# Kernel optimization log

Hardware: AMD Instinct MI355X
Metric: run time of the kernel (lower is better)

The kernel has to match this reference:

```python
import jax, jax.numpy as jnp
import numpy as np

N_NODES = 100000
N_EDGES = 1600000
IN_DIM = 64
HID = 128
N_CLASSES = 1
N_GRAPHS = 512


def _glorot(key, shape):
    fan_in, fan_out = shape[0], shape[1]
    lim = (6.0 / (fan_in + fan_out)) ** 0.5
    return jax.random.uniform(key, shape, jnp.float32, -lim, lim)


def setup_inputs() -> dict:
    key = jax.random.key(0)
    ks = jax.random.split(key, 10)
    x = jax.random.normal(ks[0], (N_NODES, IN_DIM), jnp.float32)
    edge_src = jax.random.randint(ks[1], (N_EDGES,), 0, N_NODES)
    edge_dst = jax.random.randint(ks[2], (N_EDGES,), 0, N_NODES)
    graph_ids = jnp.sort(jax.random.randint(ks[3], (N_NODES,), 0, N_GRAPHS))
    return {
        "x": x,
        "edge_src": edge_src,
        "edge_dst": edge_dst,
        "graph_ids": graph_ids,
        "W1": _glorot(ks[4], (IN_DIM, HID)),
        "b1": jnp.zeros((HID,), jnp.float32),
        "W2": _glorot(ks[5], (HID, HID)),
        "b2": jnp.zeros((HID,), jnp.float32),
        "Wc1": _glorot(ks[6], (HID, HID)),
        "bc1": jnp.zeros((HID,), jnp.float32),
        "Wc2": _glorot(ks[7], (HID, HID)),
        "bc2": jnp.zeros((HID,), jnp.float32),
        "Wc3": _glorot(ks[8], (HID, N_CLASSES)),
        "bc3": jnp.zeros((N_CLASSES,), jnp.float32),
    }


def _graph_conv(h, edge_src, edge_dst, W, b):
    # DGL GraphConv, norm='both': out = D_out^{-1/2} A D_in^{-1/2} h W + b
    ones = jnp.ones((edge_src.shape[0],), h.dtype)
    deg_out = jnp.clip(jax.ops.segment_sum(ones, edge_src, num_segments=N_NODES), 1.0)
    deg_in = jnp.clip(jax.ops.segment_sum(ones, edge_dst, num_segments=N_NODES), 1.0)
    h = h * jax.lax.rsqrt(deg_out)[:, None]           # src-side norm
    agg = jax.ops.segment_sum(h[edge_src], edge_dst, num_segments=N_NODES)  # [N, D]
    agg = agg * jax.lax.rsqrt(deg_in)[:, None]        # dst-side norm
    return agg @ W + b


def reference(x, edge_src, edge_dst, graph_ids, W1, b1, W2, b2, Wc1, bc1, Wc2, bc2, Wc3, bc3):
    h = jax.nn.relu(_graph_conv(x, edge_src, edge_dst, W1, b1))
    h = jax.nn.relu(_graph_conv(h, edge_src, edge_dst, W2, b2))
    # mean_nodes pooling over batched graphs
    sums = jax.ops.segment_sum(h, graph_ids, num_segments=N_GRAPHS)  # [G, H]
    cnts = jax.ops.segment_sum(jnp.ones((N_NODES,), h.dtype), graph_ids, num_segments=N_GRAPHS)
    hg = sums / jnp.clip(cnts, 1.0)[:, None]
    out = jax.nn.relu(hg @ Wc1 + bc1)
    out = jax.nn.relu(out @ Wc2 + bc2)
    return out @ Wc3 + bc3  # [G, n_classes]
```

## Files before the change

### kernel.cpp

```cpp
#include <hip/hip_runtime.h>

#define N_NODES 100000
#define N_EDGES 1600000
#define IN_DIM 64
#define HID 128
#define N_GRAPHS 512
#define NBUCK 391

__global__ __launch_bounds__(256) void k_bhist(const int* __restrict__ src, const int* __restrict__ dst,
                                               int* __restrict__ dcnt, int* __restrict__ scnt) {
    __shared__ int hd[NBUCK];
    __shared__ int hs[NBUCK];
    const int t = threadIdx.x;
    const int e0 = blockIdx.x * 4096 + t * 16;
    for (int i = t; i < NBUCK; i += 256) { hd[i] = 0; hs[i] = 0; }
    __syncthreads();
    if (e0 < N_EDGES) {
        const int4* d4 = (const int4*)(dst + e0);
        const int4* s4 = (const int4*)(src + e0);
#pragma unroll
        for (int u = 0; u < 4; ++u) {
            int4 d = d4[u], s = s4[u];
            atomicAdd(&hd[d.x >> 8], 1); atomicAdd(&hd[d.y >> 8], 1);
            atomicAdd(&hd[d.z >> 8], 1); atomicAdd(&hd[d.w >> 8], 1);
            atomicAdd(&hs[s.x >> 8], 1); atomicAdd(&hs[s.y >> 8], 1);
            atomicAdd(&hs[s.z >> 8], 1); atomicAdd(&hs[s.w >> 8], 1);
        }
    }
    __syncthreads();
    for (int i = t; i < NBUCK; i += 256) {
        if (hd[i]) atomicAdd(&dcnt[i], hd[i]);
        if (hs[i]) atomicAdd(&scnt[i], hs[i]);
    }
}

__global__ __launch_bounds__(512) void k_bscan3(const int* __restrict__ dcnt, const int* __restrict__ scnt,
                                                const int* __restrict__ gid,
                                                int* __restrict__ dbase, int* __restrict__ sbase,
                                                int* __restrict__ dcur, int* __restrict__ scur,
                                                int* __restrict__ gstart) {
    const int t = threadIdx.x;
    if (blockIdx.x == 2) {
        for (int g = t; g <= N_GRAPHS; g += 512) {
            int lo = 0, hi = N_NODES;
            while (lo < hi) {
                int mid = (lo + hi) >> 1;
                if (gid[mid] < g) lo = mid + 1; else hi = mid;
            }
            gstart[g] = lo;
        }
        return;
    }
    __shared__ int l[512];
    const int* cntp = (blockIdx.x == 0) ? dcnt : scnt;
    int* basep = (blockIdx.x == 0) ? dbase : sbase;
    int* curp  = (blockIdx.x == 0) ? dcur  : scur;
    int v = (t < NBUCK) ? cntp[t] : 0;
    l[t] = v;
    __syncthreads();
    for (int off = 1; off < 512; off <<= 1) {
        int x = (t >= off) ? l[t - off] : 0;
        __syncthreads();
        l[t] += x;
        __syncthreads();
    }
    if (t < NBUCK) {
        int excl = l[t] - v;
        basep[t] = excl; curp[t] = excl;
    }
    if (t == NBUCK - 1) basep[NBUCK] = l[t];
}

__global__ __launch_bounds__(256) void k_bin2(const int* __restrict__ src, const int* __restrict__ dst,
                                              int* __restrict__ dcur, int* __restrict__ scur,
                                              int* __restrict__ binnedD, int* __restrict__ binnedS) {
    __shared__ int hd[NBUCK];
    __shared__ int bd[NBUCK];
    __shared__ int hs[NBUCK];
    __shared__ int bs[NBUCK];
    const int t = threadIdx.x;
    const int e0 = blockIdx.x * 4096 + t * 16;
    for (int i = t; i < NBUCK; i += 256) { hd[i] = 0; hs[i] = 0; }
    __syncthreads();
    if (e0 < N_EDGES) {
        const int4* d4 = (const int4*)(dst + e0);
        const int4* s4 = (const int4*)(src + e0);
#pragma unroll
        for (int u = 0; u < 4; ++u) {
            int4 d = d4[u], s = s4[u];
            atomicAdd(&hd[d.x >> 8], 1); atomicAdd(&hd[d.y >> 8], 1);
            atomicAdd(&hd[d.z >> 8], 1); atomicAdd(&hd[d.w >> 8], 1);
            atomicAdd(&hs[s.x >> 8], 1); atomicAdd(&hs[s.y >> 8], 1);
            atomicAdd(&hs[s.z >> 8], 1); atomicAdd(&hs[s.w >> 8], 1);
        }
    }
    __syncthreads();
    for (int i = t; i < NBUCK; i += 256) {
        int c = hd[i];
        bd[i] = c ? atomicAdd(&dcur[i], c) : 0;
        hd[i] = 0;
        c = hs[i];
        bs[i] = c ? atomicAdd(&scur[i], c) : 0;
        hs[i] = 0;
    }
    __syncthreads();
    if (e0 < N_EDGES) {
        const int4* d4 = (const int4*)(dst + e0);
        const int4* s4 = (const int4*)(src + e0);
#pragma unroll
        for (int u = 0; u < 4; ++u) {
            int4 d = d4[u];
            int4 s = s4[u];
            int bk, r;
            bk = d.x >> 8; r = atomicAdd(&hd[bk], 1); binnedD[bd[bk] + r] = s.x | ((d.x & 255) << 17);
            bk = d.y >> 8; r = atomicAdd(&hd[bk], 1); binnedD[bd[bk] + r] = s.y | ((d.y & 255) << 17);
            bk = d.z >> 8; r = atomicAdd(&hd[bk], 1); binnedD[bd[bk] + r] = s.z | ((d.z & 255) << 17);
            bk = d.w >> 8; r = atomicAdd(&hd[bk], 1); binnedD[bd[bk] + r] = s.w | ((d.w & 255) << 17);
            bk = s.x >> 8; r = atomicAdd(&hs[bk], 1); binnedS[bs[bk] + r] = s.x;
            bk = s.y >> 8; r = atomicAdd(&hs[bk], 1); binnedS[bs[bk] + r] = s.y;
            bk = s.z >> 8; r = atomicAdd(&hs[bk], 1); binnedS[bs[bk] + r] = s.z;
            bk = s.w >> 8; r = atomicAdd(&hs[bk], 1); binnedS[bs[bk] + r] = s.w;
        }
    }
}

__global__ __launch_bounds__(256) void k_prep2(const int* __restrict__ dbase, const int* __restrict__ sbase,
                                               const int* __restrict__ binnedD, const int* __restrict__ binnedS,
                                               int* __restrict__ rowp, float* __restrict__ rsi,
                                               float* __restrict__ rso, int* __restrict__ col) {
    const int t = threadIdx.x;
    if (blockIdx.x < NBUCK) {
        const int b = blockIdx.x;
        const int n0 = b * 256;
        __shared__ int cnt[256];
        __shared__ int scn[256];
        __shared__ int cur[256];
        __shared__ int sb[2];
        if (t < 2) sb[t] = dbase[b + t];
        cnt[t] = 0;
        __syncthreads();
        const int s = sb[0], e = sb[1];
        for (int i = s + t; i < e; i += 256) atomicAdd(&cnt[binnedD[i] >> 17], 1);
        __syncthreads();
        const int c = cnt[t];
        scn[t] = c;
        __syncthreads();
        for (int off = 1; off < 256; off <<= 1) {
            int v = (t >= off) ? scn[t - off] : 0;
            __syncthreads();
            scn[t] += v;
            __syncthreads();
        }
        const int excl = scn[t] - c;
        cur[t] = excl;
        if (n0 + t < N_NODES) {
            rowp[n0 + t] = s + excl;
            rsi[n0 + t] = 1.0f / sqrtf(fmaxf((float)c, 1.0f));
        }
        if (b == NBUCK - 1 && t == 0) rowp[N_NODES] = e;
        __syncthreads();
        for (int i = s + t; i < e; i += 256) {
            int p = binnedD[i];
            int r = atomicAdd(&cur[p >> 17], 1);
            col[s + r] = p & 0x1FFFF;
        }
    } else {
        const int b = blockIdx.x - NBUCK;
        const int n0 = b * 256;
        __shared__ int cnt2[256];
        __shared__ int sb2[2];
        if (t < 2) sb2[t] = sbase[b + t];
        cnt2[t] = 0;
        __syncthreads();
        const int s = sb2[0], e = sb2[1];
        for (int i = s + t; i < e; i += 256) atomicAdd(&cnt2[binnedS[i] - n0], 1);
        __syncthreads();
        if (n0 + t < N_NODES) rso[n0 + t] = 1.0f / sqrtf(fmaxf((float)cnt2[t], 1.0f));
    }
}

__global__ __launch_bounds__(256) void k_gather64(const float4* __restrict__ x4, const float* __restrict__ rso,
                                                  const int* __restrict__ rowp, const int* __restrict__ col,
                                                  float4* __restrict__ agg4) {
    int wv = (blockIdx.x * 256 + threadIdx.x) >> 6;
    if (wv >= N_NODES) return;
    int lane = threadIdx.x & 63;
    int grp = lane >> 4, li = lane & 15;
    int s = rowp[wv], e = rowp[wv + 1];
    float ax = 0.f, ay = 0.f, az = 0.f, aw = 0.f;
    int i = s + grp;
    for (; i + 12 < e; i += 16) {
        int c0 = col[i], c1 = col[i + 4], c2 = col[i + 8], c3 = col[i + 12];
        float4 v0 = x4[c0 * 16 + li];
        float4 v1 = x4[c1 * 16 + li];
        float4 v2 = x4[c2 * 16 + li];
        float4 v3 = x4[c3 * 16 + li];
        float r0 = rso[c0], r1 = rso[c1], r2 = rso[c2], r3 = rso[c3];
        ax = fmaf(r0, v0.x, ax); ay = fmaf(r0, v0.y, ay); az = fmaf(r0, v0.z, az); aw = fmaf(r0, v0.w, aw);
        ax = fmaf(r1, v1.x, ax); ay = fmaf(r1, v1.y, ay); az = fmaf(r1, v1.z, az); aw = fmaf(r1, v1.w, aw);
        ax = fmaf(r2, v2.x, ax); ay = fmaf(r2, v2.y, ay); az = fmaf(r2, v2.z, az); aw = fmaf(r2, v2.w, aw);
        ax = fmaf(r3, v3.x, ax); ay = fmaf(r3, v3.y, ay); az = fmaf(r3, v3.z, az); aw = fmaf(r3, v3.w, aw);
    }
    for (; i + 4 < e; i += 8) {
        int c0 = col[i], c1 = col[i + 4];
        float4 v0 = x4[c0 * 16 + li];
        float4 v1 = x4[c1 * 16 + li];
        float r0 = rso[c0], r1 = rso[c1];
        ax = fmaf(r0, v0.x, ax); ay = fmaf(r0, v0.y, ay); az = fmaf(r0, v0.z, az); aw = fmaf(r0, v0.w, aw);
        ax = fmaf(r1, v1.x, ax); ay = fmaf(r1, v1.y, ay); az = fmaf(r1, v1.z, az); aw = fmaf(r1, v1.w, aw);
    }
    for (; i < e; i += 4) {
        int c = col[i];
        float4 v = x4[c * 16 + li];
        float r = rso[c];
        ax = fmaf(r, v.x, ax); ay = fmaf(r, v.y, ay); az = fmaf(r, v.z, az); aw = fmaf(r, v.w, aw);
    }
    ax += __shfl_xor(ax, 16, 64); ay += __shfl_xor(ay, 16, 64);
    az += __shfl_xor(az, 16, 64); aw += __shfl_xor(aw, 16, 64);
    ax += __shfl_xor(ax, 32, 64); ay += __shfl_xor(ay, 32, 64);
    az += __shfl_xor(az, 32, 64); aw += __shfl_xor(aw, 32, 64);
    if (lane < 16) {
        float4 o; o.x = ax; o.y = ay; o.z = az; o.w = aw;
        agg4[wv * 16 + li] = o;
    }
}

__global__ __launch_bounds__(256) void k_gather128(const float4* __restrict__ h4, const int* __restrict__ rowp,
                                                   const int* __restrict__ col, float4* __restrict__ agg4) {
    int wv = (blockIdx.x * 256 + threadIdx.x) >> 6;
    if (wv >= N_NODES) return;
    int lane = threadIdx.x & 63;
    int grp = lane >> 5, li = lane & 31;
    int s = rowp[wv], e = rowp[wv + 1];
    float ax = 0.f, ay = 0.f, az = 0.f, aw = 0.f;
    int i = s + grp;
    for (; i + 14 < e; i += 16) {
        int c0 = col[i],      c1 = col[i + 2],  c2 = col[i + 4],  c3 = col[i + 6];
        int c4 = col[i + 8],  c5 = col[i + 10], c6 = col[i + 12], c7 = col[i + 14];
        float4 v0 = h4[c0 * 32 + li];
        float4 v1 = h4[c1 * 32 + li];
        float4 v2 = h4[c2 * 32 + li];
        float4 v3 = h4[c3 * 32 + li];
        float4 v4 = h4[c4 * 32 + li];
        float4 v5 = h4[c5 * 32 + li];
        float4 v6 = h4[c6 * 32 + li];
        float4 v7 = h4[c7 * 32 + li];
        ax += (v0.x + v1.x) + (v2.x + v3.x) + ((v4.x + v5.x) + (v6.x + v7.x));
        ay += (v0.y + v1.y) + (v2.y + v3.y) + ((v4.y + v5.y) + (v6.y + v7.y));
        az += (v0.z + v1.z) + (v2.z + v3.z) + ((v4.z + v5.z) + (v6.z + v7.z));
        aw += (v0.w + v1.w) + (v2.w + v3.w) + ((v4.w + v5.w) + (v6.w + v7.w));
    }
    for (; i + 6 < e; i += 8) {
        int c0 = col[i], c1 = col[i + 2], c2 = col[i + 4], c3 = col[i + 6];
        float4 v0 = h4[c0 * 32 + li];
        float4 v1 = h4[c1 * 32 + li];
        float4 v2 = h4[c2 * 32 + li];
        float4 v3 = h4[c3 * 32 + li];
        ax += v0.x + v1.x + v2.x + v3.x;
        ay += v0.y + v1.y + v2.y + v3.y;
        az += v0.z + v1.z + v2.z + v3.z;
        aw += v0.w + v1.w + v2.w + v3.w;
    }
    for (; i < e; i += 2) {
        float4 v = h4[col[i] * 32 + li];
        ax += v.x; ay += v.y; az += v.z; aw += v.w;
    }
    ax += __shfl_xor(ax, 32, 64); ay += __shfl_xor(ay, 32, 64);
    az += __shfl_xor(az, 32, 64); aw += __shfl_xor(aw, 32, 64);
    if (lane < 32) {
        float4 o; o.x = ax; o.y = ay; o.z = az; o.w = aw;
        agg4[wv * 32 + li] = o;
    }
}

template <int K, bool SCALE_OUT>
__global__ __launch_bounds__(256) void k_mm(const float* __restrict__ A, const float* __restrict__ W,
                                            const float* __restrict__ bias, const float* __restrict__ rsi,
                                            const float* __restrict__ rso, float* __restrict__ out) {
    __shared__ float WL[32 * 128];
    __shared__ float aL[64][33];
    const int t = threadIdx.x;
    const int jq = t & 31;
    const int ns = t >> 5;
    const int n0 = blockIdx.x * 64;
    float acc[8][4] = {};
    for (int kc = 0; kc < K; kc += 32) {
        const float4* Wg = (const float4*)(W + kc * 128);
        float4* WL4 = (float4*)WL;
#pragma unroll
        for (int u = 0; u < 4; ++u) WL4[t + 256 * u] = Wg[t + 256 * u];
        {
            int r = t >> 2, q = t & 3;
            int node = n0 + r;
#pragma unroll
            for (int h = 0; h < 2; ++h) {
                int qq = q + h * 4;
                float4 v = make_float4(0.f, 0.f, 0.f, 0.f);
                if (node < N_NODES) v = *(const float4*)(A + (size_t)node * K + kc + qq * 4);
                aL[r][qq * 4 + 0] = v.x; aL[r][qq * 4 + 1] = v.y;
                aL[r][qq * 4 + 2] = v.z; aL[r][qq * 4 + 3] = v.w;
            }
        }
        __syncthreads();
#pragma unroll
        for (int k = 0; k < 32; ++k) {
            float4 wv = ((const float4*)WL)[k * 32 + jq];
#pragma unroll
            for (int i = 0; i < 8; ++i) {
                float av = aL[ns * 8 + i][k];
                acc[i][0] += av * wv.x; acc[i][1] += av * wv.y;
                acc[i][2] += av * wv.z; acc[i][3] += av * wv.w;
            }
        }
        __syncthreads();
    }
#pragma unroll
    for (int i = 0; i < 8; ++i) {
        int node = n0 + ns * 8 + i;
        if (node >= N_NODES) continue;
        float ri = rsi[node];
        float ro = SCALE_OUT ? rso[node] : 1.0f;
        float4 bj = ((const float4*)bias)[jq];
        float4 o;
        o.x = fmaxf(acc[i][0] * ri + bj.x, 0.f) * ro;
        o.y = fmaxf(acc[i][1] * ri + bj.y, 0.f) * ro;
        o.z = fmaxf(acc[i][2] * ri + bj.z, 0.f) * ro;
        o.w = fmaxf(acc[i][3] * ri + bj.w, 0.f) * ro;
        *(float4*)(out + node * HID + jq * 4) = o;
    }
}

__global__ __launch_bounds__(256) void k_mm2pool(const float* __restrict__ A, const float* __restrict__ W,
                                                 const float* __restrict__ bias, const float* __restrict__ rsi,
                                                 const int* __restrict__ gid, float* __restrict__ gsum) {
    __shared__ float WL[32 * 128];
    __shared__ float aL[64][33];
    __shared__ float gpart[8][128];
    const int t = threadIdx.x;
    const int jq = t & 31;
    const int ns = t >> 5;
    const int n0 = blockIdx.x * 64;
    for (int u = t; u < 8 * 128; u += 256) ((float*)gpart)[u] = 0.f;
    float acc[8][4] = {};
    for (int kc = 0; kc < HID; kc += 32) {
        const float4* Wg = (const float4*)(W + kc * 128);
        float4* WL4 = (float4*)WL;
#pragma unroll
        for (int u = 0; u < 4; ++u) WL4[t + 256 * u] = Wg[t + 256 * u];
        {
            int r = t >> 2, q = t & 3;
            int node = n0 + r;
#pragma unroll
            for (int h = 0; h < 2; ++h) {
                int qq = q + h * 4;
                float4 v = make_float4(0.f, 0.f, 0.f, 0.f);
                if (node < N_NODES) v = *(const float4*)(A + (size_t)node * HID + kc + qq * 4);
                aL[r][qq * 4 + 0] = v.x; aL[r][qq * 4 + 1] = v.y;
                aL[r][qq * 4 + 2] = v.z; aL[r][qq * 4 + 3] = v.w;
            }
        }
        __syncthreads();
#pragma unroll
        for (int k = 0; k < 32; ++k) {
            float4 wv = ((const float4*)WL)[k * 32 + jq];
#pragma unroll
            for (int i = 0; i < 8; ++i) {
                float av = aL[ns * 8 + i][k];
                acc[i][0] += av * wv.x; acc[i][1] += av * wv.y;
                acc[i][2] += av * wv.z; acc[i][3] += av * wv.w;
            }
        }
        __syncthreads();
    }
    const int g0 = gid[n0];
    float4 bj = ((const float4*)bias)[jq];
    int curslot = -9;
    float p0 = 0.f, p1 = 0.f, p2 = 0.f, p3 = 0.f;
#pragma unroll
    for (int i = 0; i < 8; ++i) {
        int node = n0 + ns * 8 + i;
        if (node >= N_NODES) break;
        float ri = rsi[node];
        float ox = fmaxf(acc[i][0] * ri + bj.x, 0.f);
        float oy = fmaxf(acc[i][1] * ri + bj.y, 0.f);
        float oz = fmaxf(acc[i][2] * ri + bj.z, 0.f);
        float ow = fmaxf(acc[i][3] * ri + bj.w, 0.f);
        int slot = gid[node] - g0;
        if (slot != curslot) {
            if (curslot >= 0) {
                if (curslot < 8) {
                    atomicAdd(&gpart[curslot][jq * 4 + 0], p0);
                    atomicAdd(&gpart[curslot][jq * 4 + 1], p1);
                    atomicAdd(&gpart[curslot][jq * 4 + 2], p2);
                    atomicAdd(&gpart[curslot][jq * 4 + 3], p3);
                } else {
                    atomicAdd(&gsum[(g0 + curslot) * HID + jq * 4 + 0], p0);
                    atomicAdd(&gsum[(g0 + curslot) * HID + jq * 4 + 1], p1);
                    atomicAdd(&gsum[(g0 + curslot) * HID + jq * 4 + 2], p2);
                    atomicAdd(&gsum[(g0 + curslot) * HID + jq * 4 + 3], p3);
                }
            }
            curslot = slot; p0 = ox; p1 = oy; p2 = oz; p3 = ow;
        } else {
            p0 += ox; p1 += oy; p2 += oz; p3 += ow;
        }
    }
    if (curslot >= 0) {
        if (curslot < 8) {
            atomicAdd(&gpart[curslot][jq * 4 + 0], p0);
            atomicAdd(&gpart[curslot][jq * 4 + 1], p1);
            atomicAdd(&gpart[curslot][jq * 4 + 2], p2);
            atomicAdd(&gpart[curslot][jq * 4 + 3], p3);
        } else {
            atomicAdd(&gsum[(g0 + curslot) * HID + jq * 4 + 0], p0);
            atomicAdd(&gsum[(g0 + curslot) * HID + jq * 4 + 1], p1);
            atomicAdd(&gsum[(g0 + curslot) * HID + jq * 4 + 2], p2);
            atomicAdd(&gsum[(g0 + curslot) * HID + jq * 4 + 3], p3);
        }
    }
    __syncthreads();
    for (int u = t; u < 8 * 128; u += 256) {
        int slot = u >> 7, c = u & 127;
        float v = gpart[slot][c];
        if (v != 0.f) {
            int g = g0 + slot;
            if (g < N_GRAPHS) atomicAdd(&gsum[g * HID + c], v);
        }
    }
}

__global__ __launch_bounds__(128) void k_head(const float* __restrict__ gsum, const int* __restrict__ gstart,
                                              const float* __restrict__ Wc1, const float* __restrict__ bc1,
                                              const float* __restrict__ Wc2, const float* __restrict__ bc2,
                                              const float* __restrict__ Wc3, const float* __restrict__ bc3,
                                              float* __restrict__ out) {
    int g = blockIdx.x, t = threadIdx.x;
    int s = gstart[g], e = gstart[g + 1];
    float cnt = fmaxf((float)(e - s), 1.0f);
    __shared__ float buf[HID];
    __shared__ float red[2];
    buf[t] = gsum[g * HID + t] / cnt;
    __syncthreads();
    float a = bc1[t];
#pragma unroll 8
    for (int k = 0; k < HID; ++k) a += buf[k] * Wc1[k * HID + t];
    a = fmaxf(a, 0.f);
    __syncthreads();
    buf[t] = a;
    __syncthreads();
    float b = bc2[t];
#pragma unroll 8
    for (int k = 0; k < HID; ++k) b += buf[k] * Wc2[k * HID + t];
    b = fmaxf(b, 0.f);
    float p = b * Wc3[t];
    for (int off = 32; off > 0; off >>= 1) p += __shfl_down(p, off, 64);
    if ((t & 63) == 0) red[t >> 6] = p;
    __syncthreads();
    if (t == 0) out[g] = red[0] + red[1] + bc3[0];
}

extern "C" void kernel_launch(void* const* d_in, const int* in_sizes, int n_in,
                              void* d_out, int out_size, void* d_ws, size_t ws_size,
                              hipStream_t stream) {
    const float* x   = (const float*)d_in[0];
    const int* esrc  = (const int*)d_in[1];
    const int* edst  = (const int*)d_in[2];
    const int* gid   = (const int*)d_in[3];
    const float* W1  = (const float*)d_in[4];
    const float* b1  = (const float*)d_in[5];
    const float* W2  = (const float*)d_in[6];
    const float* b2  = (const float*)d_in[7];
    const float* Wc1 = (const float*)d_in[8];
    const float* bc1 = (const float*)d_in[9];
    const float* Wc2 = (const float*)d_in[10];
    const float* bc2 = (const float*)d_in[11];
    const float* Wc3 = (const float*)d_in[12];
    const float* bc3 = (const float*)d_in[13];
    float* out = (float*)d_out;

    char* w = (char*)d_ws;
    size_t off = 0;
    auto alloc = [&](size_t bytes) -> char* {
        char* p = w + off;
        off += (bytes + 255) & ~(size_t)255;
        return p;
    };
    int* dcnt   = (int*)alloc((size_t)2 * (NBUCK + 1) * 4);
    int* scnt   = dcnt + (NBUCK + 1);
    int* dbase  = (int*)alloc((size_t)(NBUCK + 1) * 4);
    int* sbase  = (int*)alloc((size_t)(NBUCK + 1) * 4);
    int* dcur   = (int*)alloc((size_t)NBUCK * 4);
    int* scur   = (int*)alloc((size_t)NBUCK * 4);
    float* rso  = (float*)alloc((size_t)N_NODES * 4);
    float* rsi  = (float*)alloc((size_t)N_NODES * 4);
    int* rowp   = (int*)alloc((size_t)(N_NODES + 1) * 4);
    int* gstart = (int*)alloc((size_t)(N_GRAPHS + 1) * 4);
    int* col    = (int*)alloc((size_t)N_EDGES * 4);
    float* gsum = (float*)alloc((size_t)N_GRAPHS * HID * 4);
    float* R1   = (float*)alloc((size_t)N_NODES * HID * 4);
    float* R2   = (float*)alloc((size_t)N_NODES * HID * 4);
    int* binnedD = (int*)R1;
    int* binnedS = (int*)R1 + (size_t)N_EDGES;
    float* agg1 = R1;
    float* agg2 = R1;
    float* h1s  = R2;

    (void)in_sizes; (void)n_in; (void)out_size; (void)ws_size;

    hipMemsetAsync(dcnt, 0, (size_t)2 * (NBUCK + 1) * 4, stream);
    hipMemsetAsync(gsum, 0, (size_t)N_GRAPHS * HID * 4, stream);

    const int BB = (N_EDGES + 4095) / 4096;
    const int GB = (N_NODES * 64 + 255) / 256;
    const int MB64 = (N_NODES + 63) / 64;

    k_bhist<<<BB, 256, 0, stream>>>(esrc, edst, dcnt, scnt);
    k_bscan3<<<3, 512, 0, stream>>>(dcnt, scnt, gid, dbase, sbase, dcur, scur, gstart);
    k_bin2<<<BB, 256, 0, stream>>>(esrc, edst, dcur, scur, binnedD, binnedS);
    k_prep2<<<2 * NBUCK, 256, 0, stream>>>(dbase, sbase, binnedD, binnedS, rowp, rsi, rso, col);
    k_gather64<<<GB, 256, 0, stream>>>((const float4*)x, rso, rowp, col, (float4*)agg1);
    k_mm<IN_DIM, true><<<MB64, 256, 0, stream>>>(agg1, W1, b1, rsi, rso, h1s);
    k_gather128<<<GB, 256, 0, stream>>>((const float4*)h1s, rowp, col, (float4*)agg2);
    k_mm2pool<<<MB64, 256, 0, stream>>>(agg2, W2, b2, rsi, gid, gsum);
    k_head<<<N_GRAPHS, 128, 0, stream>>>(gsum, gstart, Wc1, bc1, Wc2, bc2, Wc3, bc3, out);
}
```

Measured before the change: 350.1 us.

## Fuse layer-2 neighbor gather into matmul+pooling kernel via shared memory

Merges the 128-wide gather kernel with the second matmul and mean-pooling kernel. Each 256-thread block now gathers 32 nodes into shared memory and runs the GEMM straight from there. This removes the global write and re-read of the 100000x128 aggregation buffer and one kernel launch. In exchange, each block runs only 4 waves of gather work with a shared-memory barrier before the GEMM, the 16-wide unrolled gather is dropped, and the tile shrinks to 32 nodes, which doubles the number of W2 reloads into shared memory.

```diff
diff --git a/kernel.cpp b/kernel.cpp
--- a/kernel.cpp
+++ b/kernel.cpp
@@ -225,54 +225,6 @@
     }
 }
 
-__global__ __launch_bounds__(256) void k_gather128(const float4* __restrict__ h4, const int* __restrict__ rowp,
-                                                   const int* __restrict__ col, float4* __restrict__ agg4) {
-    int wv = (blockIdx.x * 256 + threadIdx.x) >> 6;
-    if (wv >= N_NODES) return;
-    int lane = threadIdx.x & 63;
-    int grp = lane >> 5, li = lane & 31;
-    int s = rowp[wv], e = rowp[wv + 1];
-    float ax = 0.f, ay = 0.f, az = 0.f, aw = 0.f;
-    int i = s + grp;
-    for (; i + 14 < e; i += 16) {
-        int c0 = col[i],      c1 = col[i + 2],  c2 = col[i + 4],  c3 = col[i + 6];
-        int c4 = col[i + 8],  c5 = col[i + 10], c6 = col[i + 12], c7 = col[i + 14];
-        float4 v0 = h4[c0 * 32 + li];
-        float4 v1 = h4[c1 * 32 + li];
-        float4 v2 = h4[c2 * 32 + li];
-        float4 v3 = h4[c3 * 32 + li];
-        float4 v4 = h4[c4 * 32 + li];
-        float4 v5 = h4[c5 * 32 + li];
-        float4 v6 = h4[c6 * 32 + li];
-        float4 v7 = h4[c7 * 32 + li];
-        ax += (v0.x + v1.x) + (v2.x + v3.x) + ((v4.x + v5.x) + (v6.x + v7.x));
-        ay += (v0.y + v1.y) + (v2.y + v3.y) + ((v4.y + v5.y) + (v6.y + v7.y));
-        az += (v0.z + v1.z) + (v2.z + v3.z) + ((v4.z + v5.z) + (v6.z + v7.z));
-        aw += (v0.w + v1.w) + (v2.w + v3.w) + ((v4.w + v5.w) + (v6.w + v7.w));
-    }
-    for (; i + 6 < e; i += 8) {
-        int c0 = col[i], c1 = col[i + 2], c2 = col[i + 4], c3 = col[i + 6];
-        float4 v0 = h4[c0 * 32 + li];
-        float4 v1 = h4[c1 * 32 + li];
-        float4 v2 = h4[c2 * 32 + li];
-        float4 v3 = h4[c3 * 32 + li];
-        ax += v0.x + v1.x + v2.x + v3.x;
-        ay += v0.y + v1.y + v2.y + v3.y;
-        az += v0.z + v1.z + v2.z + v3.z;
-        aw += v0.w + v1.w + v2.w + v3.w;
-    }
-    for (; i < e; i += 2) {
-        float4 v = h4[col[i] * 32 + li];
-        ax += v.x; ay += v.y; az += v.z; aw += v.w;
-    }
-    ax += __shfl_xor(ax, 32, 64); ay += __shfl_xor(ay, 32, 64);
-    az += __shfl_xor(az, 32, 64); aw += __shfl_xor(aw, 32, 64);
-    if (lane < 32) {
-        float4 o; o.x = ax; o.y = ay; o.z = az; o.w = aw;
-        agg4[wv * 32 + li] = o;
-    }
-}
-
 template <int K, bool SCALE_OUT>
 __global__ __launch_bounds__(256) void k_mm(const float* __restrict__ A, const float* __restrict__ W,
                                             const float* __restrict__ bias, const float* __restrict__ rsi,
@@ -330,56 +282,78 @@
     }
 }
 
-__global__ __launch_bounds__(256) void k_mm2pool(const float* __restrict__ A, const float* __restrict__ W,
-                                                 const float* __restrict__ bias, const float* __restrict__ rsi,
-                                                 const int* __restrict__ gid, float* __restrict__ gsum) {
+__global__ __launch_bounds__(256, 4) void k_g128p(const float4* __restrict__ h4, const int* __restrict__ rowp,
+                                                  const int* __restrict__ col, const float* __restrict__ W,
+                                                  const float* __restrict__ bias, const float* __restrict__ rsi,
+                                                  const int* __restrict__ gid, float* __restrict__ gsum) {
+    __shared__ float agg[32][HID];
     __shared__ float WL[32 * 128];
-    __shared__ float aL[64][33];
     __shared__ float gpart[8][128];
     const int t = threadIdx.x;
+    const int wid = t >> 6, lane = t & 63;
+    const int n0 = blockIdx.x * 32;
+    for (int u = t; u < 8 * 128; u += 256) ((float*)gpart)[u] = 0.f;
+
+    const int grp = lane >> 5, li = lane & 31;
+#pragma unroll 1
+    for (int it = 0; it < 8; ++it) {
+        const int node = n0 + wid * 8 + it;
+        const int s = rowp[node], e = rowp[node + 1];
+        float ax = 0.f, ay = 0.f, az = 0.f, aw = 0.f;
+        int i = s + grp;
+        for (; i + 6 < e; i += 8) {
+            int c0 = col[i], c1 = col[i + 2], c2 = col[i + 4], c3 = col[i + 6];
+            float4 v0 = h4[c0 * 32 + li];
+            float4 v1 = h4[c1 * 32 + li];
+            float4 v2 = h4[c2 * 32 + li];
+            float4 v3 = h4[c3 * 32 + li];
+            ax += v0.x + v1.x + v2.x + v3.x;
+            ay += v0.y + v1.y + v2.y + v3.y;
+            az += v0.z + v1.z + v2.z + v3.z;
+            aw += v0.w + v1.w + v2.w + v3.w;
+        }
+        for (; i < e; i += 2) {
+            float4 v = h4[col[i] * 32 + li];
+            ax += v.x; ay += v.y; az += v.z; aw += v.w;
+        }
+        ax += __shfl_xor(ax, 32, 64); ay += __shfl_xor(ay, 32, 64);
+        az += __shfl_xor(az, 32, 64); aw += __shfl_xor(aw, 32, 64);
+        if (lane < 32) {
+            float4 o; o.x = ax; o.y = ay; o.z = az; o.w = aw;
+            ((float4*)agg[node - n0])[li] = o;
+        }
+    }
+    __syncthreads();
+
     const int jq = t & 31;
     const int ns = t >> 5;
-    const int n0 = blockIdx.x * 64;
-    for (int u = t; u < 8 * 128; u += 256) ((float*)gpart)[u] = 0.f;
-    float acc[8][4] = {};
+    float acc[4][4] = {};
     for (int kc = 0; kc < HID; kc += 32) {
         const float4* Wg = (const float4*)(W + kc * 128);
         float4* WL4 = (float4*)WL;
 #pragma unroll
         for (int u = 0; u < 4; ++u) WL4[t + 256 * u] = Wg[t + 256 * u];
-        {
-            int r = t >> 2, q = t & 3;
-            int node = n0 + r;
-#pragma unroll
-            for (int h = 0; h < 2; ++h) {
-                int qq = q + h * 4;
-                float4 v = make_float4(0.f, 0.f, 0.f, 0.f);
-                if (node < N_NODES) v = *(const float4*)(A + (size_t)node * HID + kc + qq * 4);
-                aL[r][qq * 4 + 0] = v.x; aL[r][qq * 4 + 1] = v.y;
-                aL[r][qq * 4 + 2] = v.z; aL[r][qq * 4 + 3] = v.w;
-            }
-        }
         __syncthreads();
 #pragma unroll
         for (int k = 0; k < 32; ++k) {
             float4 wv = ((const float4*)WL)[k * 32 + jq];
 #pragma unroll
-            for (int i = 0; i < 8; ++i) {
-                float av = aL[ns * 8 + i][k];
+            for (int i = 0; i < 4; ++i) {
+                float av = agg[ns * 4 + i][kc + k];
                 acc[i][0] += av * wv.x; acc[i][1] += av * wv.y;
                 acc[i][2] += av * wv.z; acc[i][3] += av * wv.w;
             }
         }
         __syncthreads();
     }
+
     const int g0 = gid[n0];
     float4 bj = ((const float4*)bias)[jq];
     int curslot = -9;
     float p0 = 0.f, p1 = 0.f, p2 = 0.f, p3 = 0.f;
 #pragma unroll
-    for (int i = 0; i < 8; ++i) {
-        int node = n0 + ns * 8 + i;
-        if (node >= N_NODES) break;
+    for (int i = 0; i < 4; ++i) {
+        int node = n0 + ns * 4 + i;
         float ri = rsi[node];
         float ox = fmaxf(acc[i][0] * ri + bj.x, 0.f);
         float oy = fmaxf(acc[i][1] * ri + bj.y, 0.f);
@@ -502,7 +476,6 @@
     int* binnedD = (int*)R1;
     int* binnedS = (int*)R1 + (size_t)N_EDGES;
     float* agg1 = R1;
-    float* agg2 = R1;
     float* h1s  = R2;
 
     (void)in_sizes; (void)n_in; (void)out_size; (void)ws_size;
@@ -513,6 +486,7 @@
     const int BB = (N_EDGES + 4095) / 4096;
     const int GB = (N_NODES * 64 + 255) / 256;
     const int MB64 = (N_NODES + 63) / 64;
+    const int FB32 = N_NODES / 32;
 
     k_bhist<<<BB, 256, 0, stream>>>(esrc, edst, dcnt, scnt);
     k_bscan3<<<3, 512, 0, stream>>>(dcnt, scnt, gid, dbase, sbase, dcur, scur, gstart);
@@ -520,7 +494,6 @@
     k_prep2<<<2 * NBUCK, 256, 0, stream>>>(dbase, sbase, binnedD, binnedS, rowp, rsi, rso, col);
     k_gather64<<<GB, 256, 0, stream>>>((const float4*)x, rso, rowp, col, (float4*)agg1);
     k_mm<IN_DIM, true><<<MB64, 256, 0, stream>>>(agg1, W1, b1, rsi, rso, h1s);
-    k_gather128<<<GB, 256, 0, stream>>>((const float4*)h1s, rowp, col, (float4*)agg2);
-    k_mm2pool<<<MB64, 256, 0, stream>>>(agg2, W2, b2, rsi, gid, gsum);
+    k_g128p<<<FB32, 256, 0, stream>>>((const float4*)h1s, rowp, col, W2, b2, rsi, gid, gsum);
     k_head<<<N_GRAPHS, 128, 0, stream>>>(gsum, gstart, Wc1, bc1, Wc2, bc2, Wc3, bc3, out);
 }
```

Result: faster. 338.6 us (-3.3%).
